# Kernel tuning notes

Hardware: AMD Instinct MI355X
Metric: run time of the kernel (lower is better)

The kernel has to match this reference:

```python
import jax, jax.numpy as jnp
import numpy as np

B_, DM, H_, W_ = 4, 96, 64, 64   # batch, d_inner, spatial
N_, R_, K_ = 16, 6, 4            # d_state, dt_rank, num scan directions


def setup_inputs() -> dict:
    key = jax.random.key(0)
    ks = jax.random.split(key, 16)
    nrm = lambda k, s, sc=0.1: (jax.random.normal(k, s, jnp.float32) * sc)
    A_log = jnp.log(jnp.tile(jnp.arange(1, N_ + 1, dtype=jnp.float32)[None, :], (K_ * DM, 1)))
    return {
        "x": jax.random.normal(ks[0], (B_, DM, H_, W_), jnp.float32),
        "y": jax.random.normal(ks[1], (B_, DM, H_, W_), jnp.float32),
        "x_proj_w_der": nrm(ks[2], (K_, R_ + 2 * N_, DM)),
        "dt_w_der": nrm(ks[3], (K_, DM, R_)),
        "dt_b_der": nrm(ks[4], (K_, DM), 0.5) - 3.0,
        "A_logs_der": A_log,
        "Ds_der": jnp.ones((K_ * DM,), jnp.float32),
        "x_proj_w_cli": nrm(ks[5], (K_, R_ + 2 * N_, DM)),
        "dt_w_cli": nrm(ks[6], (K_, DM, R_)),
        "dt_b_cli": nrm(ks[7], (K_, DM), 0.5) - 3.0,
        "A_logs_cli": A_log,
        "Ds_cli": jnp.ones((K_ * DM,), jnp.float32),
        "ln1_scale": jnp.ones((DM,), jnp.float32),
        "ln1_bias": jnp.zeros((DM,), jnp.float32),
        "ln2_scale": jnp.ones((DM,), jnp.float32),
        "ln2_bias": jnp.zeros((DM,), jnp.float32),
    }


def traverse_four(x, x_proj_w, dt_w, A_logs, Ds, dt_b):
    # x: [B, D, H, W] -> 4-directional cross-scan inputs
    B, D, H, W = x.shape
    L = H * W
    R = dt_w.shape[-1]
    N = A_logs.shape[-1]
    x_hw = x.reshape(B, D, L)
    x_wh = jnp.swapaxes(x, 2, 3).reshape(B, D, L)
    base = jnp.stack([x_hw, x_wh], axis=1)                     # [B,2,D,L]
    xs = jnp.concatenate([base, jnp.flip(base, -1)], axis=1)   # [B,4,D,L]
    x_dbl = jnp.einsum('bkdl,kcd->bkcl', xs, x_proj_w)         # [B,4,R+2N,L]
    dts, Bs, Cs = jnp.split(x_dbl, [R, R + N], axis=2)
    dts = jnp.einsum('bkrl,kdr->bkdl', dts, dt_w)              # [B,4,D,L]
    As = -jnp.exp(A_logs.astype(jnp.float32)).reshape(K_, D, N)
    return xs, dts, Bs, Cs, As, Ds.astype(jnp.float32).reshape(K_, D), dt_b.astype(jnp.float32)


def selective_scan(u, dts, As, Bs, Cs, Ds, dt_b):
    # u, dts: [B,K,D,L]; Bs, Cs: [B,K,N,L]; As: [K,D,N]; Ds, dt_b: [K,D]
    delta = jax.nn.softplus(dts + dt_b[None, :, :, None])
    dlt = jnp.moveaxis(delta, -1, 0)   # [L,B,K,D]
    ut = jnp.moveaxis(u, -1, 0)
    Bt = jnp.moveaxis(Bs, -1, 0)       # [L,B,K,N]
    Ct = jnp.moveaxis(Cs, -1, 0)
    B, K, D, _ = u.shape
    N = As.shape[-1]
    h0 = jnp.zeros((B, K, D, N), jnp.float32)

    def step(h, inp):
        d_t, u_t, b_t, c_t = inp
        dA = jnp.exp(d_t[..., None] * As)                      # [B,K,D,N]
        h = h * dA + (d_t * u_t)[..., None] * b_t[:, :, None, :]
        y_t = jnp.einsum('bkdn,bkn->bkd', h, c_t)
        return h, y_t

    _, ys = jax.lax.scan(step, h0, (dlt, ut, Bt, Ct))          # ys: [L,B,K,D]
    ys = jnp.moveaxis(ys, 0, -1)                               # [B,K,D,L]
    return ys + u * Ds[None, :, :, None]


def path_overlay(out_y, H, W):
    # out_y: [B,4,D,L] -> merge the 4 scan paths back to [B,H,W,D]
    B, K, D, L = out_y.shape
    inv = jnp.flip(out_y[:, 2:4], -1)
    wh = jnp.swapaxes(out_y[:, 1].reshape(B, D, W, H), 2, 3).reshape(B, D, L)
    invwh = jnp.swapaxes(inv[:, 1].reshape(B, D, W, H), 2, 3).reshape(B, D, L)
    yy = out_y[:, 0] + inv[:, 0] + wh + invwh                  # [B,D,L]
    return jnp.swapaxes(yy, 1, 2).reshape(B, H, W, D)


def layernorm(x, scale, bias, eps=1e-5):
    m = x.mean(-1, keepdims=True)
    v = x.var(-1, keepdims=True)
    return (x - m) * jax.lax.rsqrt(v + eps) * scale + bias


def reference(x, y, x_proj_w_der, dt_w_der, dt_b_der, A_logs_der, Ds_der,
              x_proj_w_cli, dt_w_cli, dt_b_cli, A_logs_cli, Ds_cli,
              ln1_scale, ln1_bias, ln2_scale, ln2_bias):
    B, C, H, W = x.shape
    xs_d, dts_d, Bs_d, Cs_d, As_d, Ds_d, b_d = traverse_four(x, x_proj_w_der, dt_w_der, A_logs_der, Ds_der, dt_b_der)
    xs_c, dts_c, Bs_c, Cs_c, As_c, Ds_c, b_c = traverse_four(y, x_proj_w_cli, dt_w_cli, A_logs_cli, Ds_cli, dt_b_cli)
    # cross: der stream uses cli's C projection and vice versa
    y_der = selective_scan(xs_d, dts_d, As_d, Bs_d, Cs_c, Ds_d, b_d)
    y_cli = selective_scan(xs_c, dts_c, As_c, Bs_c, Cs_d, Ds_c, b_c)
    y_der = path_overlay(y_der, H, W)
    y_cli = path_overlay(y_cli, H, W)
    y_der = jnp.transpose(layernorm(y_der, ln1_scale, ln1_bias), (0, 3, 1, 2))
    y_cli = jnp.transpose(layernorm(y_cli, ln2_scale, ln2_bias), (0, 3, 1, 2))
    return (y_der, y_cli)
```

## Files before the change

kernel.cpp:

```cpp
#include <hip/hip_runtime.h>
#include <hip/hip_bf16.h>
#include <math.h>

#define LTOT 4096
#define DCH  96
#define NST  16
#define RNK  6
#define CPR  38
#define KDIR 4
#define NCH  16
#define CHUNK (LTOT / NCH)

__device__ __forceinline__ int dir_idx(int k, int l) {
  int a = l >> 6, c = l & 63;
  if (k == 0) return l;
  if (k == 1) return (c << 6) + a;
  if (k == 2) return 4095 - l;
  return ((63 - c) << 6) + (63 - a);
}

template <int CTRL>
__device__ __forceinline__ float row_shl_add(float p) {
  int moved = __builtin_amdgcn_update_dpp(0, __float_as_int(p), CTRL, 0xF, 0xF, true);
  return p + __int_as_float(moved);
}

__global__ __launch_bounds__(256) void proj_kernel(
    const float* __restrict__ x, const float* __restrict__ y,
    const float* __restrict__ xw_d, const float* __restrict__ dtw_d, const float* __restrict__ dtb_d,
    const float* __restrict__ xw_c, const float* __restrict__ dtw_c, const float* __restrict__ dtb_c,
    float* __restrict__ deltaBuf, float* __restrict__ BBuf, float* __restrict__ CBuf)
{
  int l  = blockIdx.x * 256 + threadIdx.x;
  int k  = blockIdx.y;
  int sb = blockIdx.z;
  int s  = sb >> 2, b = sb & 3;

  const float* xin = s ? y     : x;
  const float* xw  = s ? xw_c  : xw_d;
  const float* dtw = s ? dtw_c : dtw_d;
  const float* dtb = s ? dtb_c : dtb_d;

  int pos = dir_idx(k, l);
  const float* xb = xin + (size_t)b * DCH * LTOT;

  float acc[CPR];
  #pragma unroll
  for (int c = 0; c < CPR; ++c) acc[c] = 0.f;

  const float* Wk = xw + k * CPR * DCH;
  for (int d = 0; d < DCH; ++d) {
    float xv = xb[(size_t)d * LTOT + pos];
    #pragma unroll
    for (int c = 0; c < CPR; ++c) acc[c] = fmaf(xv, Wk[c * DCH + d], acc[c]);
  }

  const float* dwk = dtw + k * DCH * RNK;
  const float* dbk = dtb + k * DCH;
  float* dOut = deltaBuf + ((size_t)((s * 4 + b) * KDIR + k) * DCH) * LTOT + l;
  for (int d = 0; d < DCH; ++d) {
    float t = dbk[d];
    #pragma unroll
    for (int r = 0; r < RNK; ++r) t = fmaf(acc[r], dwk[d * RNK + r], t);
    float sp = (t > 20.f) ? t : log1pf(__expf(t));
    dOut[(size_t)d * LTOT] = sp;
  }

  float* Bo = BBuf + ((size_t)((s * 4 + b) * KDIR + k) * LTOT + l) * NST;
  float* Co = CBuf + ((size_t)((s * 4 + b) * KDIR + k) * LTOT + l) * NST;
  #pragma unroll
  for (int q = 0; q < 4; ++q) {
    float4 bv = make_float4(acc[RNK + 4*q], acc[RNK + 4*q+1], acc[RNK + 4*q+2], acc[RNK + 4*q+3]);
    float4 cv = make_float4(acc[RNK+NST + 4*q], acc[RNK+NST + 4*q+1], acc[RNK+NST + 4*q+2], acc[RNK+NST + 4*q+3]);
    ((float4*)Bo)[q] = bv;
    ((float4*)Co)[q] = cv;
  }
}

__global__ __launch_bounds__(1024) void scan_kernel(
    const float* __restrict__ x, const float* __restrict__ y,
    const float* __restrict__ Alog_d, const float* __restrict__ Ds_d,
    const float* __restrict__ Alog_c, const float* __restrict__ Ds_c,
    const float* __restrict__ deltaBuf, const float* __restrict__ BBuf,
    const float* __restrict__ CBuf, float* __restrict__ yyBuf)
{
  __shared__ float yy[LTOT];
  __shared__ float xrow[LTOT];
  __shared__ float hloc[NCH][64];
  __shared__ float Pc[NCH][64];
  __shared__ float hin[NCH][64];

  int tid  = threadIdx.x;
  int c    = tid >> 6;
  int lane = tid & 63;
  int k = lane >> 4, n = lane & 15;
  int d = blockIdx.x, b = blockIdx.y, s = blockIdx.z;

  const float* xin  = s ? y      : x;
  const float* Alog = s ? Alog_c : Alog_d;
  const float* Dsp  = s ? Ds_c   : Ds_d;

  float A2 = -__expf(Alog[(k * DCH + d) * NST + n]) * 1.44269504088896341f;

  const float* xb = xin + (size_t)(b * DCH + d) * LTOT;
  {
    float4 xv = ((const float4*)xb)[tid];
    ((float4*)xrow)[tid] = xv;
    ((float4*)yy)[tid] = make_float4(0.f, 0.f, 0.f, 0.f);
  }
  __syncthreads();

  const float* dbase = deltaBuf + ((size_t)(((s * 4 + b) * KDIR + k) * DCH + d)) * LTOT;
  const float* Bbase = BBuf + ((size_t)((s * 4 + b) * KDIR + k)) * LTOT * NST;
  const float* Cbase = CBuf + ((size_t)(((1 - s) * 4 + b) * KDIR + k)) * LTOT * NST;
  const int l0beg = c * CHUNK;

  const int dpn  = (k & 2 ? -1 : 1) * (k & 1 ? 64 : 1);
  const int dpw  = (k & 1) ? ((k & 2) ? 4031 : -4031) : dpn;
  const int dpnB = dpn * 4, dpwB = dpw * 4;

  float h = 0.f, sumd = 0.f;
  {
    int posB = dir_idx(k, l0beg) * 4;
    const float* Bp = Bbase + (size_t)l0beg * NST + n;
    for (int l0 = l0beg; l0 < l0beg + CHUNK; l0 += 4) {
      float4 dv4 = *(const float4*)(dbase + l0);
      #pragma unroll
      for (int j = 0; j < 4; ++j) {
        float delta = (&dv4.x)[j];
        float Bv = Bp[j * NST];
        float u  = *(const float*)((const char*)xrow + posB);
        sumd += delta;
        h = fmaf(h, exp2f(delta * A2), delta * u * Bv);
        posB += (((l0 + j) & 63) == 63) ? dpwB : dpnB;
      }
      Bp += 4 * NST;
    }
  }
  hloc[c][lane] = h;
  Pc[c][lane]   = exp2f(A2 * sumd);
  __syncthreads();

  if (tid < 64) {
    float hh = 0.f;
    hin[0][lane] = 0.f;
    for (int cc = 1; cc < NCH; ++cc) {
      hh = fmaf(Pc[cc - 1][lane], hh, hloc[cc - 1][lane]);
      hin[cc][lane] = hh;
    }
  }
  __syncthreads();

  h = hin[c][lane];
  {
    int posB = dir_idx(k, l0beg) * 4;
    const float* Bp = Bbase + (size_t)l0beg * NST + n;
    const float* Cp = Cbase + (size_t)l0beg * NST + n;
    for (int l0 = l0beg; l0 < l0beg + CHUNK; l0 += 4) {
      float4 dv4 = *(const float4*)(dbase + l0);
      #pragma unroll
      for (int j = 0; j < 4; ++j) {
        float delta = (&dv4.x)[j];
        float Bv = Bp[j * NST];
        float Cv = Cp[j * NST];
        float u  = *(const float*)((const char*)xrow + posB);
        h = fmaf(h, exp2f(delta * A2), delta * u * Bv);
        float p = h * Cv;
        p = row_shl_add<0x108>(p);
        p = row_shl_add<0x104>(p);
        p = row_shl_add<0x102>(p);
        p = row_shl_add<0x101>(p);
        if (n == 0) {
          atomicAdd((float*)((char*)yy + posB), p);
        }
        posB += (((l0 + j) & 63) == 63) ? dpwB : dpnB;
      }
      Bp += 4 * NST;
      Cp += 4 * NST;
    }
  }
  __syncthreads();

  float Dsum = Dsp[0 * DCH + d] + Dsp[1 * DCH + d] + Dsp[2 * DCH + d] + Dsp[3 * DCH + d];
  float* out = yyBuf + (size_t)((s * 4 + b) * DCH + d) * LTOT;
  {
    float4 v  = ((const float4*)yy)[tid];
    float4 xv = ((const float4*)xrow)[tid];
    v.x = fmaf(xv.x, Dsum, v.x);
    v.y = fmaf(xv.y, Dsum, v.y);
    v.z = fmaf(xv.z, Dsum, v.z);
    v.w = fmaf(xv.w, Dsum, v.w);
    ((float4*)out)[tid] = v;
  }
}

__global__ __launch_bounds__(256) void merge_ln_kernel(
    const float* __restrict__ yyBuf,
    const float* __restrict__ ln1s, const float* __restrict__ ln1b,
    const float* __restrict__ ln2s, const float* __restrict__ ln2b,
    float* __restrict__ out)
{
  int p = blockIdx.x * 256 + threadIdx.x;
  int b = blockIdx.y, s = blockIdx.z;

  const float* base = yyBuf + ((size_t)(s * 4 + b) * DCH) * LTOT + p;
  float v[DCH];
  float m = 0.f;
  #pragma unroll
  for (int d = 0; d < DCH; ++d) { v[d] = base[(size_t)d * LTOT]; m += v[d]; }
  m *= (1.f / DCH);
  float var = 0.f;
  #pragma unroll
  for (int d = 0; d < DCH; ++d) { float t = v[d] - m; var = fmaf(t, t, var); }
  var *= (1.f / DCH);
  float r = rsqrtf(var + 1e-5f);

  const float* sc = s ? ln2s : ln1s;
  const float* bi = s ? ln2b : ln1b;
  float* ob = out + ((size_t)(s * 4 + b) * DCH) * LTOT + p;
  #pragma unroll
  for (int d = 0; d < DCH; ++d) ob[(size_t)d * LTOT] = (v[d] - m) * r * sc[d] + bi[d];
}

extern "C" void kernel_launch(void* const* d_in, const int* in_sizes, int n_in,
                              void* d_out, int out_size, void* d_ws, size_t ws_size,
                              hipStream_t stream)
{
  const float* x      = (const float*)d_in[0];
  const float* y      = (const float*)d_in[1];
  const float* xw_d   = (const float*)d_in[2];
  const float* dtw_d  = (const float*)d_in[3];
  const float* dtb_d  = (const float*)d_in[4];
  const float* Alog_d = (const float*)d_in[5];
  const float* Ds_d   = (const float*)d_in[6];
  const float* xw_c   = (const float*)d_in[7];
  const float* dtw_c  = (const float*)d_in[8];
  const float* dtb_c  = (const float*)d_in[9];
  const float* Alog_c = (const float*)d_in[10];
  const float* Ds_c   = (const float*)d_in[11];
  const float* ln1s   = (const float*)d_in[12];
  const float* ln1b   = (const float*)d_in[13];
  const float* ln2s   = (const float*)d_in[14];
  const float* ln2b   = (const float*)d_in[15];

  float* ws = (float*)d_ws;
  float* deltaBuf = ws;
  float* BBuf  = deltaBuf + (size_t)2 * 4 * KDIR * DCH * LTOT;
  float* CBuf  = BBuf + (size_t)2 * 4 * KDIR * NST * LTOT;
  float* yyBuf = CBuf + (size_t)2 * 4 * KDIR * NST * LTOT;
  float* outF  = (float*)d_out;

  dim3 pg(LTOT / 256, KDIR, 8);
  hipLaunchKernelGGL(proj_kernel, pg, dim3(256), 0, stream,
                     x, y, xw_d, dtw_d, dtb_d, xw_c, dtw_c, dtb_c,
                     deltaBuf, BBuf, CBuf);

  dim3 sg(DCH, 4, 2);
  hipLaunchKernelGGL(scan_kernel, sg, dim3(1024), 0, stream,
                     x, y, Alog_d, Ds_d, Alog_c, Ds_c,
                     deltaBuf, BBuf, CBuf, yyBuf);

  dim3 mg(LTOT / 256, 4, 2);
  hipLaunchKernelGGL(merge_ln_kernel, mg, dim3(256), 0, stream,
                     yyBuf, ln1s, ln1b, ln2s, ln2b, outF);
}
```

Before: 401.4 us.

## Store B/C projections state-major and vectorize scan loads per row

The B and C projection buffers change from [L][N] to [N][L] layout, so each scan thread can read four consecutive timesteps of its state with a float4 load instead of strided scalar loads. The scan loops are restructured per 64-element row, which lets the row-boundary jump be computed once per row instead of per step. In the second pass the four cross-lane reductions and atomic adds are grouped after the four recurrence steps to expose more instruction-level parallelism. The cost is that the projection kernel's B/C stores become 16 scalar strided writes per thread (coalesced across threads) instead of float4 writes.

```diff
diff --git a/kernel.cpp b/kernel.cpp
--- a/kernel.cpp
+++ b/kernel.cpp
@@ -23,6 +23,13 @@
 __device__ __forceinline__ float row_shl_add(float p) {
   int moved = __builtin_amdgcn_update_dpp(0, __float_as_int(p), CTRL, 0xF, 0xF, true);
   return p + __int_as_float(moved);
+}
+__device__ __forceinline__ float reduce16(float p) {
+  p = row_shl_add<0x108>(p);
+  p = row_shl_add<0x104>(p);
+  p = row_shl_add<0x102>(p);
+  p = row_shl_add<0x101>(p);
+  return p;
 }
 
 __global__ __launch_bounds__(256) void proj_kernel(
@@ -66,14 +73,12 @@
     dOut[(size_t)d * LTOT] = sp;
   }
 
-  float* Bo = BBuf + ((size_t)((s * 4 + b) * KDIR + k) * LTOT + l) * NST;
-  float* Co = CBuf + ((size_t)((s * 4 + b) * KDIR + k) * LTOT + l) * NST;
-  #pragma unroll
-  for (int q = 0; q < 4; ++q) {
-    float4 bv = make_float4(acc[RNK + 4*q], acc[RNK + 4*q+1], acc[RNK + 4*q+2], acc[RNK + 4*q+3]);
-    float4 cv = make_float4(acc[RNK+NST + 4*q], acc[RNK+NST + 4*q+1], acc[RNK+NST + 4*q+2], acc[RNK+NST + 4*q+3]);
-    ((float4*)Bo)[q] = bv;
-    ((float4*)Co)[q] = cv;
+  float* Bo = BBuf + ((size_t)((s * 4 + b) * KDIR + k) * NST) * LTOT + l;
+  float* Co = CBuf + ((size_t)((s * 4 + b) * KDIR + k) * NST) * LTOT + l;
+  #pragma unroll
+  for (int nn = 0; nn < NST; ++nn) {
+    Bo[(size_t)nn * LTOT] = acc[RNK + nn];
+    Co[(size_t)nn * LTOT] = acc[RNK + NST + nn];
   }
 }
 
@@ -111,8 +116,8 @@
   __syncthreads();
 
   const float* dbase = deltaBuf + ((size_t)(((s * 4 + b) * KDIR + k) * DCH + d)) * LTOT;
-  const float* Bbase = BBuf + ((size_t)((s * 4 + b) * KDIR + k)) * LTOT * NST;
-  const float* Cbase = CBuf + ((size_t)(((1 - s) * 4 + b) * KDIR + k)) * LTOT * NST;
+  const float* Brow  = BBuf + ((size_t)((s * 4 + b) * KDIR + k) * NST + n) * LTOT;
+  const float* Crow  = CBuf + ((size_t)(((1 - s) * 4 + b) * KDIR + k) * NST + n) * LTOT;
   const int l0beg = c * CHUNK;
 
   const int dpn  = (k & 2 ? -1 : 1) * (k & 1 ? 64 : 1);
@@ -122,19 +127,23 @@
   float h = 0.f, sumd = 0.f;
   {
     int posB = dir_idx(k, l0beg) * 4;
-    const float* Bp = Bbase + (size_t)l0beg * NST + n;
-    for (int l0 = l0beg; l0 < l0beg + CHUNK; l0 += 4) {
-      float4 dv4 = *(const float4*)(dbase + l0);
+    for (int row = 0; row < CHUNK / 64; ++row) {
+      const float* dr = dbase + l0beg + row * 64;
+      const float* br = Brow  + l0beg + row * 64;
       #pragma unroll
-      for (int j = 0; j < 4; ++j) {
-        float delta = (&dv4.x)[j];
-        float Bv = Bp[j * NST];
-        float u  = *(const float*)((const char*)xrow + posB);
-        sumd += delta;
-        h = fmaf(h, exp2f(delta * A2), delta * u * Bv);
-        posB += (((l0 + j) & 63) == 63) ? dpwB : dpnB;
+      for (int g = 0; g < 16; ++g) {
+        float4 dv = ((const float4*)dr)[g];
+        float4 bv = ((const float4*)br)[g];
+        { float u = *(const float*)((const char*)xrow + posB);
+          sumd += dv.x; h = fmaf(h, exp2f(dv.x * A2), dv.x * u * bv.x); posB += dpnB; }
+        { float u = *(const float*)((const char*)xrow + posB);
+          sumd += dv.y; h = fmaf(h, exp2f(dv.y * A2), dv.y * u * bv.y); posB += dpnB; }
+        { float u = *(const float*)((const char*)xrow + posB);
+          sumd += dv.z; h = fmaf(h, exp2f(dv.z * A2), dv.z * u * bv.z); posB += dpnB; }
+        { float u = *(const float*)((const char*)xrow + posB);
+          sumd += dv.w; h = fmaf(h, exp2f(dv.w * A2), dv.w * u * bv.w);
+          posB += (g == 15) ? dpwB : dpnB; }
       }
-      Bp += 4 * NST;
     }
   }
   hloc[c][lane] = h;
@@ -154,29 +163,43 @@
   h = hin[c][lane];
   {
     int posB = dir_idx(k, l0beg) * 4;
-    const float* Bp = Bbase + (size_t)l0beg * NST + n;
-    const float* Cp = Cbase + (size_t)l0beg * NST + n;
-    for (int l0 = l0beg; l0 < l0beg + CHUNK; l0 += 4) {
-      float4 dv4 = *(const float4*)(dbase + l0);
+    for (int row = 0; row < CHUNK / 64; ++row) {
+      const float* dr = dbase + l0beg + row * 64;
+      const float* br = Brow  + l0beg + row * 64;
+      const float* cr = Crow  + l0beg + row * 64;
       #pragma unroll
-      for (int j = 0; j < 4; ++j) {
-        float delta = (&dv4.x)[j];
-        float Bv = Bp[j * NST];
-        float Cv = Cp[j * NST];
-        float u  = *(const float*)((const char*)xrow + posB);
-        h = fmaf(h, exp2f(delta * A2), delta * u * Bv);
-        float p = h * Cv;
-        p = row_shl_add<0x108>(p);
-        p = row_shl_add<0x104>(p);
-        p = row_shl_add<0x102>(p);
-        p = row_shl_add<0x101>(p);
+      for (int g = 0; g < 16; ++g) {
+        float4 dv = ((const float4*)dr)[g];
+        float4 bv = ((const float4*)br)[g];
+        float4 cv = ((const float4*)cr)[g];
+        int q0 = posB;
+        float u0 = *(const float*)((const char*)xrow + q0);
+        h = fmaf(h, exp2f(dv.x * A2), dv.x * u0 * bv.x);
+        float p0 = h * cv.x;
+        int q1 = q0 + dpnB;
+        float u1 = *(const float*)((const char*)xrow + q1);
+        h = fmaf(h, exp2f(dv.y * A2), dv.y * u1 * bv.y);
+        float p1 = h * cv.y;
+        int q2 = q1 + dpnB;
+        float u2 = *(const float*)((const char*)xrow + q2);
+        h = fmaf(h, exp2f(dv.z * A2), dv.z * u2 * bv.z);
+        float p2 = h * cv.z;
+        int q3 = q2 + dpnB;
+        float u3 = *(const float*)((const char*)xrow + q3);
+        h = fmaf(h, exp2f(dv.w * A2), dv.w * u3 * bv.w);
+        float p3 = h * cv.w;
+        posB = q3 + ((g == 15) ? dpwB : dpnB);
+        p0 = reduce16(p0);
+        p1 = reduce16(p1);
+        p2 = reduce16(p2);
+        p3 = reduce16(p3);
         if (n == 0) {
-          atomicAdd((float*)((char*)yy + posB), p);
+          atomicAdd((float*)((char*)yy + q0), p0);
+          atomicAdd((float*)((char*)yy + q1), p1);
+          atomicAdd((float*)((char*)yy + q2), p2);
+          atomicAdd((float*)((char*)yy + q3), p3);
         }
-        posB += (((l0 + j) & 63) == 63) ? dpwB : dpnB;
       }
-      Bp += 4 * NST;
-      Cp += 4 * NST;
     }
   }
   __syncthreads();
```

Measured after the change: 685.8 us. 1.71x slower.
